# Optimization experiments

Measured on AMD Instinct MI355X. Metric: run time of the kernel, lower is better.

Reference implementation:

```python
import jax, jax.numpy as jnp
import numpy as np

D_MODEL = 512
D_STATE = 16
D_CONV = 4
EXPAND = 2
D_INNER = EXPAND * D_MODEL          # 1024
DT_RANK = D_MODEL // 16             # 32 (canonical 'auto' dt_rank)
EPS = 1e-5


def setup_inputs() -> dict:
    key = jax.random.key(0)
    ks = jax.random.split(key, 12)
    w = lambda i, shape, s=0.02: (jax.random.normal(ks[i], shape, jnp.float32) * s)
    inp = {
        "x": jax.random.normal(ks[0], (2, 1024, D_MODEL), jnp.float32),
        # pre-mixer LayerNorm
        "ln1_g": jnp.ones((D_MODEL,), jnp.float32),
        "ln1_b": jnp.zeros((D_MODEL,), jnp.float32),
        # Mamba SSM params
        "in_proj_w": w(1, (2 * D_INNER, D_MODEL)),
        "conv_w": w(2, (D_INNER, D_CONV), 0.1),
        "conv_b": jnp.zeros((D_INNER,), jnp.float32),
        "x_proj_w": w(3, (DT_RANK + 2 * D_STATE, D_INNER)),
        "dt_proj_w": w(4, (D_INNER, DT_RANK), 0.1),
        "dt_proj_b": w(5, (D_INNER,), 0.1),
        "A_log": jnp.log(jnp.broadcast_to(
            jnp.arange(1, D_STATE + 1, dtype=jnp.float32), (D_INNER, D_STATE))),
        "D": jnp.ones((D_INNER,), jnp.float32),
        "out_proj_w": w(6, (D_MODEL, D_INNER)),
        # FFN sub-block
        "ln2_g": jnp.ones((D_MODEL,), jnp.float32),
        "ln2_b": jnp.zeros((D_MODEL,), jnp.float32),
        "ffn1_w": w(7, (4 * D_MODEL, D_MODEL)),
        "ffn1_b": jnp.zeros((4 * D_MODEL,), jnp.float32),
        "ffn2_w": w(8, (D_MODEL, 4 * D_MODEL)),
        "ffn2_b": jnp.zeros((D_MODEL,), jnp.float32),
    }
    return inp


def _layernorm(x, g, b):
    mu = jnp.mean(x, axis=-1, keepdims=True)
    var = jnp.var(x, axis=-1, keepdims=True)
    return (x - mu) * jax.lax.rsqrt(var + EPS) * g + b


def _mamba(x, in_proj_w, conv_w, conv_b, x_proj_w, dt_proj_w, dt_proj_b,
           A_log, D, out_proj_w):
    B, L, _ = x.shape
    # input projection -> (x_in, gate z), each [B, L, E]
    xz = jnp.einsum('bld,ed->ble', x, in_proj_w)
    xi, z = jnp.split(xz, 2, axis=-1)
    # depthwise causal conv1d (width D_CONV): left-pad, cross-correlate
    xp = jnp.pad(xi, ((0, 0), (D_CONV - 1, 0), (0, 0)))
    xc = conv_b
    for k in range(D_CONV):
        xc = xc + xp[:, k:k + L, :] * conv_w[:, k]
    xc = jax.nn.silu(xc)  # [B, L, E]
    # data-dependent SSM parameters
    x_dbl = jnp.einsum('ble,re->blr', xc, x_proj_w)
    dt, Bc, Cc = jnp.split(x_dbl, [DT_RANK, DT_RANK + D_STATE], axis=-1)
    delta = jax.nn.softplus(jnp.einsum('blr,er->ble', dt, dt_proj_w) + dt_proj_b)
    A = -jnp.exp(A_log)  # [E, N]
    # discretize: deltaA, deltaBx both [B, L, E, N]
    deltaA = jnp.exp(delta[..., None] * A)
    deltaBx = delta[..., None] * Bc[:, :, None, :] * xc[..., None]

    def step(h, inputs):
        dA, dBx, C = inputs                       # [B,E,N],[B,E,N],[B,N]
        h = dA * h + dBx
        y = jnp.einsum('ben,bn->be', h, C)
        return h, y

    h0 = jnp.zeros((B, D_INNER, D_STATE), x.dtype)
    _, ys = jax.lax.scan(step, h0,
                         (jnp.swapaxes(deltaA, 0, 1),
                          jnp.swapaxes(deltaBx, 0, 1),
                          jnp.swapaxes(Cc, 0, 1)))
    y = jnp.swapaxes(ys, 0, 1) + xc * D           # [B, L, E]
    y = y * jax.nn.silu(z)
    return jnp.einsum('ble,de->bld', y, out_proj_w)


def reference(x, ln1_g, ln1_b, in_proj_w, conv_w, conv_b, x_proj_w,
              dt_proj_w, dt_proj_b, A_log, D, out_proj_w,
              ln2_g, ln2_b, ffn1_w, ffn1_b, ffn2_w, ffn2_b):
    # pre-norm Mamba mixer + residual (dropout = identity in eval mode)
    h = _mamba(_layernorm(x, ln1_g, ln1_b), in_proj_w, conv_w, conv_b,
               x_proj_w, dt_proj_w, dt_proj_b, A_log, D, out_proj_w)
    x = x + h
    # pre-norm FFN + residual
    f = _layernorm(x, ln2_g, ln2_b)
    f = jax.nn.gelu(jnp.einsum('bld,fd->blf', f, ffn1_w) + ffn1_b)
    f = jnp.einsum('blf,df->bld', f, ffn2_w) + ffn2_b
    return x + f
```

## Files before the change

kernel.cpp:

```cpp
#include <hip/hip_runtime.h>
#include <cmath>

typedef unsigned short u16;
typedef __attribute__((ext_vector_type(8))) short bf16x8;
typedef __attribute__((ext_vector_type(4))) float f32x4;

#define BB    2
#define LSEQ  1024
#define DM    512
#define DI    1024
#define NTOK  2048
#define NC    64
#define CL    16

__device__ __forceinline__ float siluf(float x) {
    return x * (1.0f / (1.0f + __expf(-x)));
}
__device__ __forceinline__ float geluf(float x) {
    float c = 0.7978845608028654f * (x + 0.044715f * x * x * x);
    return 0.5f * x * (1.0f + tanhf(c));
}
__device__ __forceinline__ u16 f2bf(float f) {
    union { float f; unsigned u; } v; v.f = f;
    unsigned r = v.u + 0x7fff + ((v.u >> 16) & 1);
    return (u16)(r >> 16);
}
__device__ __forceinline__ float bf2f(u16 u) {
    union { unsigned u; float f; } v; v.u = ((unsigned)u) << 16; return v.f;
}
__device__ __forceinline__ void async_cp16(const u16* g, u16* l) {
    __builtin_amdgcn_global_load_lds(
        (const __attribute__((address_space(1))) void*)g,
        (__attribute__((address_space(3))) void*)l, 16, 0, 0);
}

#define NCVT 3680

__global__ void prep_kernel(const float* __restrict__ s0, u16* __restrict__ d0,
                            const float* __restrict__ s1, u16* __restrict__ d1,
                            const float* __restrict__ s2, u16* __restrict__ d2,
                            const float* __restrict__ s3, u16* __restrict__ d3,
                            const float* __restrict__ s4, u16* __restrict__ d4,
                            const float* __restrict__ s5, u16* __restrict__ d5,
                            const float* __restrict__ x, const float* __restrict__ g,
                            const float* __restrict__ b, u16* __restrict__ lnb)
{
    __shared__ float shs[4], shq[4];
    __shared__ float smu, srs;
    if (blockIdx.x < NCVT) {
        int i = (blockIdx.x * 256 + threadIdx.x) * 4;
        const float* sp; u16* dp; int off;
        if      (i < 1048576) { sp = s0; dp = d0; off = i; }
        else if (i < 1572864) { sp = s1; dp = d1; off = i - 1048576; }
        else if (i < 2621440) { sp = s2; dp = d2; off = i - 1572864; }
        else if (i < 3670016) { sp = s3; dp = d3; off = i - 2621440; }
        else if (i < 3735552) { sp = s4; dp = d4; off = i - 3670016; }
        else                  { sp = s5; dp = d5; off = i - 3735552; }
        float4 v = *(const float4*)(sp + off);
        ushort4 o;
        o.x = f2bf(v.x); o.y = f2bf(v.y); o.z = f2bf(v.z); o.w = f2bf(v.w);
        *(ushort4*)(dp + off) = o;
        return;
    }
    int t = blockIdx.x - NCVT;
    int tid = threadIdx.x;
    const float* xr = x + (size_t)t * DM;
    float v0 = xr[tid];
    float v1 = xr[tid + 256];
    float rsum = v0 + v1;
    float rsq  = v0 * v0 + v1 * v1;
    #pragma unroll
    for (int o = 32; o > 0; o >>= 1) { rsum += __shfl_down(rsum, o); rsq += __shfl_down(rsq, o); }
    int wid = tid >> 6, lane = tid & 63;
    if (lane == 0) { shs[wid] = rsum; shq[wid] = rsq; }
    __syncthreads();
    if (tid == 0) {
        float a  = shs[0] + shs[1] + shs[2] + shs[3];
        float a2 = shq[0] + shq[1] + shq[2] + shq[3];
        float mu = a / DM;
        float var = a2 / DM - mu * mu;
        smu = mu;
        srs = rsqrtf(var + 1e-5f);
    }
    __syncthreads();
    float mu = smu, rs = srs;
    u16* orow = lnb + (size_t)t * DM;
    orow[tid]       = f2bf((v0 - mu) * rs * g[tid]       + b[tid]);
    orow[tid + 256] = f2bf((v1 - mu) * rs * g[tid + 256] + b[tid + 256]);
}

__global__ void ln_bf16_kernel(const float* __restrict__ x, const float* __restrict__ g,
                               const float* __restrict__ b, u16* __restrict__ out)
{
    int t = blockIdx.x;
    int tid = threadIdx.x;
    const float* xr = x + (size_t)t * DM;
    float v0 = xr[tid];
    float v1 = xr[tid + 256];
    float rsum = v0 + v1;
    float rsq  = v0 * v0 + v1 * v1;
    #pragma unroll
    for (int o = 32; o > 0; o >>= 1) { rsum += __shfl_down(rsum, o); rsq += __shfl_down(rsq, o); }
    __shared__ float shs[4], shq[4];
    __shared__ float smu, srs;
    int wid = tid >> 6, lane = tid & 63;
    if (lane == 0) { shs[wid] = rsum; shq[wid] = rsq; }
    __syncthreads();
    if (tid == 0) {
        float a  = shs[0] + shs[1] + shs[2] + shs[3];
        float a2 = shq[0] + shq[1] + shq[2] + shq[3];
        float mu = a / DM;
        float var = a2 / DM - mu * mu;
        smu = mu;
        srs = rsqrtf(var + 1e-5f);
    }
    __syncthreads();
    float mu = smu, rs = srs;
    u16* orow = out + (size_t)t * DM;
    orow[tid]       = f2bf((v0 - mu) * rs * g[tid]       + b[tid]);
    orow[tid + 256] = f2bf((v1 - mu) * rs * g[tid + 256] + b[tid + 256]);
}

template<int EPI, int BM, int BN, int BK, int OBF>
__global__ __launch_bounds__(256)
void mgemm_kernel(const u16* __restrict__ A, const u16* __restrict__ W, int K,
                  void* __restrict__ Cp, int ldc,
                  const float* __restrict__ bias, const float* __restrict__ resid, int ldr)
{
    __shared__ u16 As[BM * BK];
    __shared__ u16 Bs[BN * BK];
    constexpr int WR = BM / 2, WC = BN / 2;
    constexpr int MR = WR / 16, NR = WC / 16;
    constexpr int LPR = BK / 8;
    constexpr int CH_ROWS = 64 / LPR;
    constexpr int NCH_A = BM / CH_ROWS, NCH_B = BN / CH_ROWS;

    const int tid = threadIdx.x;
    const int wave = tid >> 6, lane = tid & 63;
    const int wm = wave >> 1, wn = wave & 1;
    const int m0 = blockIdx.y * BM, n0 = blockIdx.x * BN;
    const int crow = lane / LPR, ckoff = (lane % LPR) * 8;
    const int fr = lane & 15;

    f32x4 acc[MR][NR] = {};

    for (int k0 = 0; k0 < K; k0 += BK) {
        for (int c = wave; c < NCH_A; c += 4)
            async_cp16(A + (size_t)(m0 + c * CH_ROWS + crow) * K + k0 + ckoff, &As[c * 512]);
        for (int c = wave; c < NCH_B; c += 4)
            async_cp16(W + (size_t)(n0 + c * CH_ROWS + crow) * K + k0 + ckoff, &Bs[c * 512]);
        __syncthreads();
        #pragma unroll
        for (int ks = 0; ks < BK / 32; ++ks) {
            const int fk = ks * 32 + ((lane >> 4) << 3);
            bf16x8 af[MR], bv[NR];
            #pragma unroll
            for (int i = 0; i < MR; ++i)
                af[i] = *(const bf16x8*)&As[(wm * WR + i * 16 + fr) * BK + fk];
            #pragma unroll
            for (int j = 0; j < NR; ++j)
                bv[j] = *(const bf16x8*)&Bs[(wn * WC + j * 16 + fr) * BK + fk];
            #pragma unroll
            for (int i = 0; i < MR; ++i)
                #pragma unroll
                for (int j = 0; j < NR; ++j)
                    acc[i][j] = __builtin_amdgcn_mfma_f32_16x16x32_bf16(af[i], bv[j], acc[i][j], 0, 0, 0);
        }
        __syncthreads();
    }

    const int rbase = (lane >> 4) << 2;
    #pragma unroll
    for (int i = 0; i < MR; ++i) {
        #pragma unroll
        for (int j = 0; j < NR; ++j) {
            const int col  = n0 + wn * WC + j * 16 + fr;
            const int row0 = m0 + wm * WR + i * 16 + rbase;
            float bvv = (EPI == 1 || EPI == 2 || EPI == 4) ? bias[col] : 0.0f;
            #pragma unroll
            for (int r = 0; r < 4; ++r) {
                float v = acc[i][j][r];
                if (EPI == 1) { v += bvv; v = (v < 20.0f) ? log1pf(__expf(v)) : v; }
                if (EPI == 2) v = geluf(v + bvv);
                if (EPI == 3) v += resid[(size_t)(row0 + r) * ldr + col];
                if (EPI == 4) v += bvv + resid[(size_t)(row0 + r) * ldr + col];
                if (OBF) ((u16*)Cp)[(size_t)(row0 + r) * ldc + col] = f2bf(v);
                else     ((float*)Cp)[(size_t)(row0 + r) * ldc + col] = v;
            }
        }
    }
}

template<int EPI, int OBF>
__global__ __launch_bounds__(512)
void mgemm8_kernel(const u16* __restrict__ A, const u16* __restrict__ W, int K,
                   void* __restrict__ Cp, int ldc, const float* __restrict__ bias)
{
    constexpr int BM = 128, BN = 128, BK = 64;
    __shared__ u16 As[BM * BK];
    __shared__ u16 Bs[BN * BK];
    const int tid = threadIdx.x;
    const int wave = tid >> 6, lane = tid & 63;
    const int wm = wave >> 2, wn = wave & 3;
    const int m0 = blockIdx.y * BM, n0 = blockIdx.x * BN;
    const int crow = lane >> 3, ckoff = (lane & 7) * 8;
    const int fr = lane & 15;

    f32x4 acc[4][2] = {};

    for (int k0 = 0; k0 < K; k0 += BK) {
        #pragma unroll
        for (int c = wave; c < 16; c += 8)
            async_cp16(A + (size_t)(m0 + c * 8 + crow) * K + k0 + ckoff, &As[c * 512]);
        #pragma unroll
        for (int c = wave; c < 16; c += 8)
            async_cp16(W + (size_t)(n0 + c * 8 + crow) * K + k0 + ckoff, &Bs[c * 512]);
        __syncthreads();
        #pragma unroll
        for (int ks = 0; ks < 2; ++ks) {
            const int fk = ks * 32 + ((lane >> 4) << 3);
            bf16x8 af[4], bv[2];
            #pragma unroll
            for (int i = 0; i < 4; ++i)
                af[i] = *(const bf16x8*)&As[(wm * 64 + i * 16 + fr) * BK + fk];
            #pragma unroll
            for (int j = 0; j < 2; ++j)
                bv[j] = *(const bf16x8*)&Bs[(wn * 32 + j * 16 + fr) * BK + fk];
            #pragma unroll
            for (int i = 0; i < 4; ++i)
                #pragma unroll
                for (int j = 0; j < 2; ++j)
                    acc[i][j] = __builtin_amdgcn_mfma_f32_16x16x32_bf16(af[i], bv[j], acc[i][j], 0, 0, 0);
        }
        __syncthreads();
    }

    const int rbase = (lane >> 4) << 2;
    #pragma unroll
    for (int i = 0; i < 4; ++i) {
        #pragma unroll
        for (int j = 0; j < 2; ++j) {
            const int col  = n0 + wn * 32 + j * 16 + fr;
            const int row0 = m0 + wm * 64 + i * 16 + rbase;
            float bvv = (EPI == 2) ? bias[col] : 0.0f;
            #pragma unroll
            for (int r = 0; r < 4; ++r) {
                float v = acc[i][j][r];
                if (EPI == 2) v = geluf(v + bvv);
                if (OBF) ((u16*)Cp)[(size_t)(row0 + r) * ldc + col] = f2bf(v);
                else     ((float*)Cp)[(size_t)(row0 + r) * ldc + col] = v;
            }
        }
    }
}

__global__ __launch_bounds__(256)
void xproj_part_kernel(const u16* __restrict__ A, const u16* __restrict__ W,
                       float* __restrict__ P)
{
    constexpr int BM = 64, BK = 128;
    __shared__ u16 As[BM * BK];
    __shared__ u16 Bs[64 * BK];
    const int tid = threadIdx.x;
    const int wave = tid >> 6, lane = tid & 63;
    const int wm = wave >> 1, wn = wave & 1;
    const int ks = blockIdx.x;
    const int m0 = blockIdx.y * BM;
    const int k0 = ks * BK;
    const int crow = lane >> 4, ckoff = (lane & 15) * 8;
    const int fr = lane & 15;

    for (int c = wave; c < 16; c += 4) {
        async_cp16(A + (size_t)(m0 + c * 4 + crow) * 1024 + k0 + ckoff, &As[c * 512]);
        async_cp16(W + (size_t)(c * 4 + crow) * 1024 + k0 + ckoff, &Bs[c * 512]);
    }
    __syncthreads();

    f32x4 acc[2][2] = {};
    #pragma unroll
    for (int ks2 = 0; ks2 < 4; ++ks2) {
        const int fk = ks2 * 32 + ((lane >> 4) << 3);
        bf16x8 af[2], bv[2];
        #pragma unroll
        for (int i = 0; i < 2; ++i)
            af[i] = *(const bf16x8*)&As[(wm * 32 + i * 16 + fr) * BK + fk];
        #pragma unroll
        for (int j = 0; j < 2; ++j)
            bv[j] = *(const bf16x8*)&Bs[(wn * 32 + j * 16 + fr) * BK + fk];
        #pragma unroll
        for (int i = 0; i < 2; ++i)
            #pragma unroll
            for (int j = 0; j < 2; ++j)
                acc[i][j] = __builtin_amdgcn_mfma_f32_16x16x32_bf16(af[i], bv[j], acc[i][j], 0, 0, 0);
    }

    const int rbase = (lane >> 4) << 2;
    float* Pk = P + (size_t)ks * NTOK * 64;
    #pragma unroll
    for (int i = 0; i < 2; ++i)
        #pragma unroll
        for (int j = 0; j < 2; ++j) {
            const int col  = wn * 32 + j * 16 + fr;
            const int row0 = m0 + wm * 32 + i * 16 + rbase;
            #pragma unroll
            for (int r = 0; r < 4; ++r)
                Pk[(size_t)(row0 + r) * 64 + col] = acc[i][j][r];
        }
}

__global__ void xproj_reduce_kernel(const float* __restrict__ P, float* __restrict__ xdbl,
                                    u16* __restrict__ dtb)
{
    int i = blockIdx.x * 256 + threadIdx.x;
    float s = 0.0f;
    #pragma unroll
    for (int ks = 0; ks < 8; ++ks) s += P[(size_t)ks * NTOK * 64 + i];
    xdbl[i] = s;
    int col = i & 63;
    if (col < 32) dtb[(i >> 6) * 32 + col] = f2bf(s);
}

__global__ void conv_silu_kernel(const u16* __restrict__ xz,
                                 const float* __restrict__ cw,
                                 const float* __restrict__ cb,
                                 u16* __restrict__ xcb)
{
    int idx = blockIdx.x * 256 + threadIdx.x;
    int e8 = idx & (DI / 8 - 1);
    int e  = e8 * 8;
    int t  = idx >> 7;
    int l  = t & (LSEQ - 1);
    const u16* base = xz + (size_t)t * 2048 + e;
    bf16x8 r0 = {}, r1 = {}, r2 = {}, r3;
    r3 = *(const bf16x8*)(base);
    if (l >= 1) r2 = *(const bf16x8*)(base - 2048);
    if (l >= 2) r1 = *(const bf16x8*)(base - 2 * 2048);
    if (l >= 3) r0 = *(const bf16x8*)(base - 3 * 2048);
    float o[8];
    #pragma unroll
    for (int j = 0; j < 8; ++j) {
        const float4 w = *(const float4*)(cw + (e + j) * 4);
        float acc = cb[e + j];
        acc = fmaf(bf2f((u16)r0[j]), w.x, acc);
        acc = fmaf(bf2f((u16)r1[j]), w.y, acc);
        acc = fmaf(bf2f((u16)r2[j]), w.z, acc);
        acc = fmaf(bf2f((u16)r3[j]), w.w, acc);
        o[j] = siluf(acc);
    }
    bf16x8 obf;
    #pragma unroll
    for (int j = 0; j < 8; ++j) obf[j] = (short)f2bf(o[j]);
    *(bf16x8*)(xcb + (size_t)t * DI + e) = obf;
}

__global__ void scanA_kernel(const float* __restrict__ delta,
                             const u16* __restrict__ xcb,
                             const float* __restrict__ xdbl,
                             const float* __restrict__ A_log,
                             float* __restrict__ qbuf,
                             float* __restrict__ sumd)
{
    int i = blockIdx.x * 256 + threadIdx.x;
    int e = i & (DI - 1);
    int c = (i >> 10) & (NC - 1);
    int b = i >> 16;
    float Ae[16], h[16];
    #pragma unroll
    for (int n = 0; n < 16; ++n) { Ae[n] = -__expf(A_log[e * 16 + n]); h[n] = 0.0f; }
    float sd = 0.0f;
    int l0 = c * CL;
    for (int l = 0; l < CL; ++l) {
        size_t tok = (size_t)b * LSEQ + l0 + l;
        float d   = delta[tok * DI + e];
        float xcv = bf2f(xcb[tok * DI + e]);
        sd += d;
        float dx = d * xcv;
        const float4* B4 = (const float4*)(xdbl + tok * 64 + 32);
        #pragma unroll
        for (int q = 0; q < 4; ++q) {
            float4 Bq = B4[q];
            h[4*q+0] = __expf(d * Ae[4*q+0]) * h[4*q+0] + dx * Bq.x;
            h[4*q+1] = __expf(d * Ae[4*q+1]) * h[4*q+1] + dx * Bq.y;
            h[4*q+2] = __expf(d * Ae[4*q+2]) * h[4*q+2] + dx * Bq.z;
            h[4*q+3] = __expf(d * Ae[4*q+3]) * h[4*q+3] + dx * Bq.w;
        }
    }
    size_t base = ((size_t)(b * DI + e) * NC + c) * 16;
    #pragma unroll
    for (int n = 0; n < 16; ++n) qbuf[base + n] = h[n];
    sumd[(size_t)(b * DI + e) * NC + c] = sd;
}

__global__ void scanB_kernel(const float* __restrict__ qbuf,
                             const float* __restrict__ sumd,
                             const float* __restrict__ A_log,
                             float* __restrict__ hin)
{
    int i = blockIdx.x * 256 + threadIdx.x;
    int n = i & 15;
    int e = (i >> 4) & (DI - 1);
    int b = i >> 14;
    float Ae = -__expf(A_log[e * 16 + n]);
    float h = 0.0f;
    size_t base = (size_t)(b * DI + e) * NC;
    for (int c = 0; c < NC; ++c) {
        hin[(base + c) * 16 + n] = h;
        float P = __expf(Ae * sumd[base + c]);
        h = P * h + qbuf[(base + c) * 16 + n];
    }
}

__global__ void scanC_kernel(const float* __restrict__ delta,
                             const u16* __restrict__ xcb,
                             const float* __restrict__ xdbl,
                             const u16* __restrict__ xz,
                             const float* __restrict__ A_log,
                             const float* __restrict__ Dp,
                             const float* __restrict__ hin,
                             u16* __restrict__ y)
{
    int i = blockIdx.x * 256 + threadIdx.x;
    int e = i & (DI - 1);
    int c = (i >> 10) & (NC - 1);
    int b = i >> 16;
    float Ae[16], h[16];
    size_t base = ((size_t)(b * DI + e) * NC + c) * 16;
    #pragma unroll
    for (int n = 0; n < 16; ++n) {
        Ae[n] = -__expf(A_log[e * 16 + n]);
        h[n] = hin[base + n];
    }
    float Dv = Dp[e];
    int l0 = c * CL;
    for (int l = 0; l < CL; ++l) {
        size_t tok = (size_t)b * LSEQ + l0 + l;
        float d   = delta[tok * DI + e];
        float xcv = bf2f(xcb[tok * DI + e]);
        float zv  = bf2f(xz[tok * 2048 + DI + e]);
        float dx = d * xcv;
        const float4* B4 = (const float4*)(xdbl + tok * 64 + 32);
        const float4* C4 = (const float4*)(xdbl + tok * 64 + 48);
        float yv = 0.0f;
        #pragma unroll
        for (int q = 0; q < 4; ++q) {
            float4 Bq = B4[q];
            float4 Cq = C4[q];
            float hb;
            hb = __expf(d * Ae[4*q+0]) * h[4*q+0] + dx * Bq.x; h[4*q+0] = hb; yv = fmaf(hb, Cq.x, yv);
            hb = __expf(d * Ae[4*q+1]) * h[4*q+1] + dx * Bq.y; h[4*q+1] = hb; yv = fmaf(hb, Cq.y, yv);
            hb = __expf(d * Ae[4*q+2]) * h[4*q+2] + dx * Bq.z; h[4*q+2] = hb; yv = fmaf(hb, Cq.z, yv);
            hb = __expf(d * Ae[4*q+3]) * h[4*q+3] + dx * Bq.w; h[4*q+3] = hb; yv = fmaf(hb, Cq.w, yv);
        }
        yv += xcv * Dv;
        yv *= siluf(zv);
        y[tok * DI + e] = f2bf(yv);
    }
}

extern "C" void kernel_launch(void* const* d_in, const int* in_sizes, int n_in,
                              void* d_out, int out_size, void* d_ws, size_t ws_size,
                              hipStream_t stream)
{
    const float* x         = (const float*)d_in[0];
    const float* ln1_g     = (const float*)d_in[1];
    const float* ln1_b     = (const float*)d_in[2];
    const float* in_proj_w = (const float*)d_in[3];
    const float* conv_w    = (const float*)d_in[4];
    const float* conv_b    = (const float*)d_in[5];
    const float* x_proj_w  = (const float*)d_in[6];
    const float* dt_proj_w = (const float*)d_in[7];
    const float* dt_proj_b = (const float*)d_in[8];
    const float* A_log     = (const float*)d_in[9];
    const float* Dp        = (const float*)d_in[10];
    const float* out_proj_w= (const float*)d_in[11];
    const float* ln2_g     = (const float*)d_in[12];
    const float* ln2_b     = (const float*)d_in[13];
    const float* ffn1_w    = (const float*)d_in[14];
    const float* ffn1_b    = (const float*)d_in[15];
    const float* ffn2_w    = (const float*)d_in[16];
    const float* ffn2_b    = (const float*)d_in[17];
    float* out = (float*)d_out;

    char* wsb = (char*)d_ws;
    u16*   lnb   = (u16*)wsb;    wsb += (size_t)2048 * 512 * 2;
    u16*   xzb   = (u16*)wsb;    wsb += (size_t)2048 * 2048 * 2;
    u16*   xcb   = (u16*)wsb;    wsb += (size_t)2048 * 1024 * 2;
    float* xdbl  = (float*)wsb;  wsb += (size_t)2048 * 64 * 4;
    u16*   dtb   = (u16*)wsb;    wsb += (size_t)2048 * 32 * 2;
    float* delta = (float*)wsb;  wsb += (size_t)2048 * 1024 * 4;
    float* Ppart = (float*)wsb;  wsb += (size_t)8 * 2048 * 64 * 4;
    float* qbuf  = (float*)wsb;  wsb += (size_t)2048 * NC * 16 * 4;
    float* sumd  = (float*)wsb;  wsb += (size_t)BB * DI * NC * 4;
    float* hin   = (float*)wsb;  wsb += (size_t)2048 * NC * 16 * 4;
    u16*   ybuf  = (u16*)wsb;    wsb += (size_t)2048 * 1024 * 2;
    float* x2    = (float*)wsb;  wsb += (size_t)2048 * 512 * 4;
    u16*   ffnm  = (u16*)wsb;    wsb += (size_t)2048 * 2048 * 2;
    u16*   w_in  = (u16*)wsb;    wsb += (size_t)2048 * 512 * 2;
    u16*   w_out = (u16*)wsb;    wsb += (size_t)512 * 1024 * 2;
    u16*   w_f1  = (u16*)wsb;    wsb += (size_t)2048 * 512 * 2;
    u16*   w_f2  = (u16*)wsb;    wsb += (size_t)512 * 2048 * 2;
    u16*   w_x   = (u16*)wsb;    wsb += (size_t)64 * 1024 * 2;
    u16*   w_dt  = (u16*)wsb;    wsb += (size_t)1024 * 32 * 2;

    prep_kernel<<<NCVT + NTOK, 256, 0, stream>>>(in_proj_w, w_in, out_proj_w, w_out,
                                                 ffn1_w, w_f1, ffn2_w, w_f2,
                                                 x_proj_w, w_x, dt_proj_w, w_dt,
                                                 x, ln1_g, ln1_b, lnb);
    mgemm8_kernel<0,1><<<dim3(16,16), 512, 0, stream>>>(lnb, w_in, 512, xzb, 2048, nullptr);
    conv_silu_kernel<<<(NTOK * DI) / (256 * 8), 256, 0, stream>>>(xzb, conv_w, conv_b, xcb);
    xproj_part_kernel<<<dim3(8, 32), 256, 0, stream>>>(xcb, w_x, Ppart);
    xproj_reduce_kernel<<<(NTOK * 64) / 256, 256, 0, stream>>>(Ppart, xdbl, dtb);
    mgemm_kernel<1,128,128,32,0><<<dim3(8,16), 256, 0, stream>>>(dtb, w_dt, 32, delta, 1024, dt_proj_b, nullptr, 0);
    scanA_kernel<<<(BB * NC * DI) / 256, 256, 0, stream>>>(delta, xcb, xdbl, A_log, qbuf, sumd);
    scanB_kernel<<<(BB * DI * 16) / 256, 256, 0, stream>>>(qbuf, sumd, A_log, hin);
    scanC_kernel<<<(BB * NC * DI) / 256, 256, 0, stream>>>(delta, xcb, xdbl, xzb, A_log, Dp, hin, ybuf);
    mgemm_kernel<3,64,64,128,0><<<dim3(8,32), 256, 0, stream>>>(ybuf, w_out, 1024, x2, 512, nullptr, x, 512);
    ln_bf16_kernel<<<NTOK, 256, 0, stream>>>(x2, ln2_g, ln2_b, lnb);
    mgemm8_kernel<2,1><<<dim3(16,16), 512, 0, stream>>>(lnb, w_f1, 512, ffnm, 2048, ffn1_b);
    mgemm_kernel<4,64,64,128,0><<<dim3(8,32), 256, 0, stream>>>(ffnm, w_f2, 2048, out, 512, ffn2_b, x2, 512);
}
```

Before: 186.9 us.

## Fuse dt projection and three-pass chunked scan into one wave-level scan kernel

Replaces the dt_proj GEMM and the three scan kernels (chunk-local, carry propagation, and final output) with a single kernel. In it, one wavefront owns a (batch, channel) pair and each lane owns a 16-token chunk. The dt projection and softplus are computed inline per token, and chunk carries are combined with a shuffle-based prefix scan across the wavefront. This removes the fp32 delta buffer, the qbuf/hin/sumd intermediates and three launches. In exchange, per-lane global reads are now strided by chunk rather than coalesced across channels, and the dt and B/C rows are re-read for every channel.

New measurement: 229.1 us. 22.6% more time.

```diff
diff --git a/kernel.cpp b/kernel.cpp
--- a/kernel.cpp
+++ b/kernel.cpp
@@ -10,7 +10,6 @@
 #define DM    512
 #define DI    1024
 #define NTOK  2048
-#define NC    64
 #define CL    16
 
 __device__ __forceinline__ float siluf(float x) {
@@ -176,12 +175,10 @@
         for (int j = 0; j < NR; ++j) {
             const int col  = n0 + wn * WC + j * 16 + fr;
             const int row0 = m0 + wm * WR + i * 16 + rbase;
-            float bvv = (EPI == 1 || EPI == 2 || EPI == 4) ? bias[col] : 0.0f;
+            float bvv = (EPI == 4) ? bias[col] : 0.0f;
             #pragma unroll
             for (int r = 0; r < 4; ++r) {
                 float v = acc[i][j][r];
-                if (EPI == 1) { v += bvv; v = (v < 20.0f) ? log1pf(__expf(v)) : v; }
-                if (EPI == 2) v = geluf(v + bvv);
                 if (EPI == 3) v += resid[(size_t)(row0 + r) * ldr + col];
                 if (EPI == 4) v += bvv + resid[(size_t)(row0 + r) * ldr + col];
                 if (OBF) ((u16*)Cp)[(size_t)(row0 + r) * ldc + col] = f2bf(v);
@@ -353,91 +350,85 @@
     *(bf16x8*)(xcb + (size_t)t * DI + e) = obf;
 }
 
-__global__ void scanA_kernel(const float* __restrict__ delta,
-                             const u16* __restrict__ xcb,
-                             const float* __restrict__ xdbl,
-                             const float* __restrict__ A_log,
-                             float* __restrict__ qbuf,
-                             float* __restrict__ sumd)
-{
-    int i = blockIdx.x * 256 + threadIdx.x;
-    int e = i & (DI - 1);
-    int c = (i >> 10) & (NC - 1);
-    int b = i >> 16;
-    float Ae[16], h[16];
-    #pragma unroll
-    for (int n = 0; n < 16; ++n) { Ae[n] = -__expf(A_log[e * 16 + n]); h[n] = 0.0f; }
-    float sd = 0.0f;
-    int l0 = c * CL;
+__global__ __launch_bounds__(256)
+void scan_fused_kernel(const u16* __restrict__ dtb,
+                       const u16* __restrict__ wdt,
+                       const float* __restrict__ dt_bias,
+                       const u16* __restrict__ xcb,
+                       const float* __restrict__ xdbl,
+                       const u16* __restrict__ xz,
+                       const float* __restrict__ A_log,
+                       const float* __restrict__ Dp,
+                       u16* __restrict__ y)
+{
+    const int gw   = (blockIdx.x * 256 + threadIdx.x) >> 6;
+    const int lane = threadIdx.x & 63;
+    const int b = gw >> 10;
+    const int e = gw & (DI - 1);
+
+    float Ae[16];
+    #pragma unroll
+    for (int n = 0; n < 16; ++n) Ae[n] = -__expf(A_log[e * 16 + n]);
+    const float Dv = Dp[e];
+    const float dbias = dt_bias[e];
+    bf16x8 wv[4];
+    #pragma unroll
+    for (int q = 0; q < 4; ++q) wv[q] = *(const bf16x8*)(wdt + e * 32 + q * 8);
+
+    const int t0 = b * LSEQ + lane * CL;
+
+    float d[CL], xc[CL], h[16];
+    #pragma unroll
+    for (int n = 0; n < 16; ++n) h[n] = 0.0f;
+    float sumd = 0.0f;
+    #pragma unroll
     for (int l = 0; l < CL; ++l) {
-        size_t tok = (size_t)b * LSEQ + l0 + l;
-        float d   = delta[tok * DI + e];
+        const size_t tok = (size_t)(t0 + l);
+        float dt = dbias;
+        const u16* dr = dtb + tok * 32;
+        #pragma unroll
+        for (int q = 0; q < 4; ++q) {
+            bf16x8 dv = *(const bf16x8*)(dr + q * 8);
+            #pragma unroll
+            for (int k = 0; k < 8; ++k)
+                dt = fmaf(bf2f((u16)dv[k]), bf2f((u16)wv[q][k]), dt);
+        }
+        float dd = (dt < 20.0f) ? log1pf(__expf(dt)) : dt;
+        d[l] = dd;
+        sumd += dd;
         float xcv = bf2f(xcb[tok * DI + e]);
-        sd += d;
-        float dx = d * xcv;
+        xc[l] = xcv;
+        float dx = dd * xcv;
         const float4* B4 = (const float4*)(xdbl + tok * 64 + 32);
         #pragma unroll
         for (int q = 0; q < 4; ++q) {
             float4 Bq = B4[q];
-            h[4*q+0] = __expf(d * Ae[4*q+0]) * h[4*q+0] + dx * Bq.x;
-            h[4*q+1] = __expf(d * Ae[4*q+1]) * h[4*q+1] + dx * Bq.y;
-            h[4*q+2] = __expf(d * Ae[4*q+2]) * h[4*q+2] + dx * Bq.z;
-            h[4*q+3] = __expf(d * Ae[4*q+3]) * h[4*q+3] + dx * Bq.w;
-        }
-    }
-    size_t base = ((size_t)(b * DI + e) * NC + c) * 16;
-    #pragma unroll
-    for (int n = 0; n < 16; ++n) qbuf[base + n] = h[n];
-    sumd[(size_t)(b * DI + e) * NC + c] = sd;
-}
-
-__global__ void scanB_kernel(const float* __restrict__ qbuf,
-                             const float* __restrict__ sumd,
-                             const float* __restrict__ A_log,
-                             float* __restrict__ hin)
-{
-    int i = blockIdx.x * 256 + threadIdx.x;
-    int n = i & 15;
-    int e = (i >> 4) & (DI - 1);
-    int b = i >> 14;
-    float Ae = -__expf(A_log[e * 16 + n]);
-    float h = 0.0f;
-    size_t base = (size_t)(b * DI + e) * NC;
-    for (int c = 0; c < NC; ++c) {
-        hin[(base + c) * 16 + n] = h;
-        float P = __expf(Ae * sumd[base + c]);
-        h = P * h + qbuf[(base + c) * 16 + n];
-    }
-}
-
-__global__ void scanC_kernel(const float* __restrict__ delta,
-                             const u16* __restrict__ xcb,
-                             const float* __restrict__ xdbl,
-                             const u16* __restrict__ xz,
-                             const float* __restrict__ A_log,
-                             const float* __restrict__ Dp,
-                             const float* __restrict__ hin,
-                             u16* __restrict__ y)
-{
-    int i = blockIdx.x * 256 + threadIdx.x;
-    int e = i & (DI - 1);
-    int c = (i >> 10) & (NC - 1);
-    int b = i >> 16;
-    float Ae[16], h[16];
-    size_t base = ((size_t)(b * DI + e) * NC + c) * 16;
+            h[4*q+0] = __expf(dd * Ae[4*q+0]) * h[4*q+0] + dx * Bq.x;
+            h[4*q+1] = __expf(dd * Ae[4*q+1]) * h[4*q+1] + dx * Bq.y;
+            h[4*q+2] = __expf(dd * Ae[4*q+2]) * h[4*q+2] + dx * Bq.z;
+            h[4*q+3] = __expf(dd * Ae[4*q+3]) * h[4*q+3] + dx * Bq.w;
+        }
+    }
+
     #pragma unroll
     for (int n = 0; n < 16; ++n) {
-        Ae[n] = -__expf(A_log[e * 16 + n]);
-        h[n] = hin[base + n];
-    }
-    float Dv = Dp[e];
-    int l0 = c * CL;
+        float A  = __expf(Ae[n] * sumd);
+        float Bv = h[n];
+        #pragma unroll
+        for (int off = 1; off < 64; off <<= 1) {
+            float Ap = __shfl_up(A, off);
+            float Bp = __shfl_up(Bv, off);
+            if (lane >= off) { Bv = fmaf(A, Bp, Bv); A *= Ap; }
+        }
+        float pe = __shfl_up(Bv, 1);
+        h[n] = (lane == 0) ? 0.0f : pe;
+    }
+
+    #pragma unroll
     for (int l = 0; l < CL; ++l) {
-        size_t tok = (size_t)b * LSEQ + l0 + l;
-        float d   = delta[tok * DI + e];
-        float xcv = bf2f(xcb[tok * DI + e]);
-        float zv  = bf2f(xz[tok * 2048 + DI + e]);
-        float dx = d * xcv;
+        const size_t tok = (size_t)(t0 + l);
+        const float dd = d[l], xcv = xc[l];
+        const float dx = dd * xcv;
         const float4* B4 = (const float4*)(xdbl + tok * 64 + 32);
         const float4* C4 = (const float4*)(xdbl + tok * 64 + 48);
         float yv = 0.0f;
@@ -446,13 +437,13 @@
             float4 Bq = B4[q];
             float4 Cq = C4[q];
             float hb;
-            hb = __expf(d * Ae[4*q+0]) * h[4*q+0] + dx * Bq.x; h[4*q+0] = hb; yv = fmaf(hb, Cq.x, yv);
-            hb = __expf(d * Ae[4*q+1]) * h[4*q+1] + dx * Bq.y; h[4*q+1] = hb; yv = fmaf(hb, Cq.y, yv);
-            hb = __expf(d * Ae[4*q+2]) * h[4*q+2] + dx * Bq.z; h[4*q+2] = hb; yv = fmaf(hb, Cq.z, yv);
-            hb = __expf(d * Ae[4*q+3]) * h[4*q+3] + dx * Bq.w; h[4*q+3] = hb; yv = fmaf(hb, Cq.w, yv);
+            hb = __expf(dd * Ae[4*q+0]) * h[4*q+0] + dx * Bq.x; h[4*q+0] = hb; yv = fmaf(hb, Cq.x, yv);
+            hb = __expf(dd * Ae[4*q+1]) * h[4*q+1] + dx * Bq.y; h[4*q+1] = hb; yv = fmaf(hb, Cq.y, yv);
+            hb = __expf(dd * Ae[4*q+2]) * h[4*q+2] + dx * Bq.z; h[4*q+2] = hb; yv = fmaf(hb, Cq.z, yv);
+            hb = __expf(dd * Ae[4*q+3]) * h[4*q+3] + dx * Bq.w; h[4*q+3] = hb; yv = fmaf(hb, Cq.w, yv);
         }
         yv += xcv * Dv;
-        yv *= siluf(zv);
+        yv *= siluf(bf2f(xz[tok * 2048 + DI + e]));
         y[tok * DI + e] = f2bf(yv);
     }
 }
@@ -487,11 +478,7 @@
     u16*   xcb   = (u16*)wsb;    wsb += (size_t)2048 * 1024 * 2;
     float* xdbl  = (float*)wsb;  wsb += (size_t)2048 * 64 * 4;
     u16*   dtb   = (u16*)wsb;    wsb += (size_t)2048 * 32 * 2;
-    float* delta = (float*)wsb;  wsb += (size_t)2048 * 1024 * 4;
     float* Ppart = (float*)wsb;  wsb += (size_t)8 * 2048 * 64 * 4;
-    float* qbuf  = (float*)wsb;  wsb += (size_t)2048 * NC * 16 * 4;
-    float* sumd  = (float*)wsb;  wsb += (size_t)BB * DI * NC * 4;
-    float* hin   = (float*)wsb;  wsb += (size_t)2048 * NC * 16 * 4;
     u16*   ybuf  = (u16*)wsb;    wsb += (size_t)2048 * 1024 * 2;
     float* x2    = (float*)wsb;  wsb += (size_t)2048 * 512 * 4;
     u16*   ffnm  = (u16*)wsb;    wsb += (size_t)2048 * 2048 * 2;
@@ -510,10 +497,8 @@
     conv_silu_kernel<<<(NTOK * DI) / (256 * 8), 256, 0, stream>>>(xzb, conv_w, conv_b, xcb);
     xproj_part_kernel<<<dim3(8, 32), 256, 0, stream>>>(xcb, w_x, Ppart);
     xproj_reduce_kernel<<<(NTOK * 64) / 256, 256, 0, stream>>>(Ppart, xdbl, dtb);
-    mgemm_kernel<1,128,128,32,0><<<dim3(8,16), 256, 0, stream>>>(dtb, w_dt, 32, delta, 1024, dt_proj_b, nullptr, 0);
-    scanA_kernel<<<(BB * NC * DI) / 256, 256, 0, stream>>>(delta, xcb, xdbl, A_log, qbuf, sumd);
-    scanB_kernel<<<(BB * DI * 16) / 256, 256, 0, stream>>>(qbuf, sumd, A_log, hin);
-    scanC_kernel<<<(BB * NC * DI) / 256, 256, 0, stream>>>(delta, xcb, xdbl, xzb, A_log, Dp, hin, ybuf);
+    scan_fused_kernel<<<NTOK / 4, 256, 0, stream>>>(dtb, w_dt, dt_proj_b, xcb, xdbl,
+                                                    xzb, A_log, Dp, ybuf);
     mgemm_kernel<3,64,64,128,0><<<dim3(8,32), 256, 0, stream>>>(ybuf, w_out, 1024, x2, 512, nullptr, x, 512);
     ln_bf16_kernel<<<NTOK, 256, 0, stream>>>(x2, ln2_g, ln2_b, lnb);
     mgemm8_kernel<2,1><<<dim3(16,16), 512, 0, stream>>>(lnb, w_f1, 512, ffnm, 2048, ffn1_b);
```

## Fuse dt_proj and softplus into scan kernels, drop delta buffer

Applied to the files above, without the earlier changes.

Removes the separate dt_proj GEMM that wrote an fp32 delta tensor of 2048x1024, and instead recomputes delta inside scanA and scanC with a 32-element dot product of the bf16 dt row against per-channel weights held in registers. This cuts one launch and the write plus two reads of the 8 MB delta tensor. In exchange every scan thread does 32 extra FMAs and a softplus per token, twice across the two scan passes. The dt row reads are the same for all threads of a wave, so they broadcast. The unused EPI 1 and 2 epilogue code is removed from mgemm_kernel.

New measurement: 171.7 us. 1.09x faster.

```diff
diff --git a/kernel.cpp b/kernel.cpp
--- a/kernel.cpp
+++ b/kernel.cpp
@@ -176,12 +176,10 @@
         for (int j = 0; j < NR; ++j) {
             const int col  = n0 + wn * WC + j * 16 + fr;
             const int row0 = m0 + wm * WR + i * 16 + rbase;
-            float bvv = (EPI == 1 || EPI == 2 || EPI == 4) ? bias[col] : 0.0f;
+            float bvv = (EPI == 4) ? bias[col] : 0.0f;
             #pragma unroll
             for (int r = 0; r < 4; ++r) {
                 float v = acc[i][j][r];
-                if (EPI == 1) { v += bvv; v = (v < 20.0f) ? log1pf(__expf(v)) : v; }
-                if (EPI == 2) v = geluf(v + bvv);
                 if (EPI == 3) v += resid[(size_t)(row0 + r) * ldr + col];
                 if (EPI == 4) v += bvv + resid[(size_t)(row0 + r) * ldr + col];
                 if (OBF) ((u16*)Cp)[(size_t)(row0 + r) * ldc + col] = f2bf(v);
@@ -353,7 +351,24 @@
     *(bf16x8*)(xcb + (size_t)t * DI + e) = obf;
 }
 
-__global__ void scanA_kernel(const float* __restrict__ delta,
+__device__ __forceinline__ float delta_of(const u16* __restrict__ dtb, size_t tok,
+                                          const bf16x8* wv, float dbias)
+{
+    float dt = dbias;
+    const u16* dr = dtb + tok * 32;
+    #pragma unroll
+    for (int q = 0; q < 4; ++q) {
+        bf16x8 dv = *(const bf16x8*)(dr + q * 8);
+        #pragma unroll
+        for (int k = 0; k < 8; ++k)
+            dt = fmaf(bf2f((u16)dv[k]), bf2f((u16)wv[q][k]), dt);
+    }
+    return (dt < 20.0f) ? log1pf(__expf(dt)) : dt;
+}
+
+__global__ void scanA_kernel(const u16* __restrict__ dtb,
+                             const u16* __restrict__ wdt,
+                             const float* __restrict__ dt_bias,
                              const u16* __restrict__ xcb,
                              const float* __restrict__ xdbl,
                              const float* __restrict__ A_log,
@@ -367,11 +382,15 @@
     float Ae[16], h[16];
     #pragma unroll
     for (int n = 0; n < 16; ++n) { Ae[n] = -__expf(A_log[e * 16 + n]); h[n] = 0.0f; }
+    const float dbias = dt_bias[e];
+    bf16x8 wv[4];
+    #pragma unroll
+    for (int q = 0; q < 4; ++q) wv[q] = *(const bf16x8*)(wdt + e * 32 + q * 8);
     float sd = 0.0f;
     int l0 = c * CL;
     for (int l = 0; l < CL; ++l) {
         size_t tok = (size_t)b * LSEQ + l0 + l;
-        float d   = delta[tok * DI + e];
+        float d = delta_of(dtb, tok, wv, dbias);
         float xcv = bf2f(xcb[tok * DI + e]);
         sd += d;
         float dx = d * xcv;
@@ -410,7 +429,9 @@
     }
 }
 
-__global__ void scanC_kernel(const float* __restrict__ delta,
+__global__ void scanC_kernel(const u16* __restrict__ dtb,
+                             const u16* __restrict__ wdt,
+                             const float* __restrict__ dt_bias,
                              const u16* __restrict__ xcb,
                              const float* __restrict__ xdbl,
                              const u16* __restrict__ xz,
@@ -430,11 +451,15 @@
         Ae[n] = -__expf(A_log[e * 16 + n]);
         h[n] = hin[base + n];
     }
+    const float dbias = dt_bias[e];
+    bf16x8 wv[4];
+    #pragma unroll
+    for (int q = 0; q < 4; ++q) wv[q] = *(const bf16x8*)(wdt + e * 32 + q * 8);
     float Dv = Dp[e];
     int l0 = c * CL;
     for (int l = 0; l < CL; ++l) {
         size_t tok = (size_t)b * LSEQ + l0 + l;
-        float d   = delta[tok * DI + e];
+        float d = delta_of(dtb, tok, wv, dbias);
         float xcv = bf2f(xcb[tok * DI + e]);
         float zv  = bf2f(xz[tok * 2048 + DI + e]);
         float dx = d * xcv;
@@ -487,7 +512,6 @@
     u16*   xcb   = (u16*)wsb;    wsb += (size_t)2048 * 1024 * 2;
     float* xdbl  = (float*)wsb;  wsb += (size_t)2048 * 64 * 4;
     u16*   dtb   = (u16*)wsb;    wsb += (size_t)2048 * 32 * 2;
-    float* delta = (float*)wsb;  wsb += (size_t)2048 * 1024 * 4;
     float* Ppart = (float*)wsb;  wsb += (size_t)8 * 2048 * 64 * 4;
     float* qbuf  = (float*)wsb;  wsb += (size_t)2048 * NC * 16 * 4;
     float* sumd  = (float*)wsb;  wsb += (size_t)BB * DI * NC * 4;
@@ -510,10 +534,9 @@
     conv_silu_kernel<<<(NTOK * DI) / (256 * 8), 256, 0, stream>>>(xzb, conv_w, conv_b, xcb);
     xproj_part_kernel<<<dim3(8, 32), 256, 0, stream>>>(xcb, w_x, Ppart);
     xproj_reduce_kernel<<<(NTOK * 64) / 256, 256, 0, stream>>>(Ppart, xdbl, dtb);
-    mgemm_kernel<1,128,128,32,0><<<dim3(8,16), 256, 0, stream>>>(dtb, w_dt, 32, delta, 1024, dt_proj_b, nullptr, 0);
-    scanA_kernel<<<(BB * NC * DI) / 256, 256, 0, stream>>>(delta, xcb, xdbl, A_log, qbuf, sumd);
+    scanA_kernel<<<(BB * NC * DI) / 256, 256, 0, stream>>>(dtb, w_dt, dt_proj_b, xcb, xdbl, A_log, qbuf, sumd);
     scanB_kernel<<<(BB * DI * 16) / 256, 256, 0, stream>>>(qbuf, sumd, A_log, hin);
-    scanC_kernel<<<(BB * NC * DI) / 256, 256, 0, stream>>>(delta, xcb, xdbl, xzb, A_log, Dp, hin, ybuf);
+    scanC_kernel<<<(BB * NC * DI) / 256, 256, 0, stream>>>(dtb, w_dt, dt_proj_b, xcb, xdbl, xzb, A_log, Dp, hin, ybuf);
     mgemm_kernel<3,64,64,128,0><<<dim3(8,32), 256, 0, stream>>>(ybuf, w_out, 1024, x2, 512, nullptr, x, 512);
     ln_bf16_kernel<<<NTOK, 256, 0, stream>>>(x2, ln2_g, ln2_b, lnb);
     mgemm8_kernel<2,1><<<dim3(16,16), 512, 0, stream>>>(lnb, w_f1, 512, ffnm, 2048, ffn1_b);
```
